# Performance work log

Hardware: AMD Instinct MI355X
Metric: run time of the kernel (lower is better)

## Reference

```python
import jax, jax.numpy as jnp
import numpy as np

B, H, S, D = 2, 16, 2048, 128

def setup_inputs() -> dict:
    key = jax.random.key(0)
    k1, k2, k3, k4 = jax.random.split(key, 4)
    queries = jax.random.normal(k1, (B, H, S, D), dtype=jnp.float32)
    keys = jax.random.normal(k2, (B, H, S, D), dtype=jnp.float32)
    values = jax.random.normal(k3, (B, H, S, D), dtype=jnp.float32)
    mask = jax.random.randint(k4, (B, 1, S, S), 0, 2).astype(jnp.int32)
    return {"queries": queries, "keys": keys, "values": values, "d_k": D, "mask": mask}

def reference(queries, keys, values, d_k, mask):
    # scores: [B, H, S, S]
    scale = 1.0 / jnp.sqrt(jnp.float32(d_k))
    scores = jnp.einsum('bhqd,bhkd->bhqk', queries, keys) * scale
    if mask is not None:
        scores = scores + (-1e9) * mask.astype(scores.dtype)
    weights = jax.nn.softmax(scores, axis=-1)
    out = jnp.einsum('bhqk,bhkd->bhqd', weights, values)
    return out
```

## Files before the change

kernel.cpp:

```cpp
#include <hip/hip_runtime.h>
#include <hip/hip_bf16.h>

#define BB 2
#define HH 16
#define SS 2048
#define DD 128
#define QBLK 128
#define KVBLK 64
#define NT (SS / KVBLK)
#define TILE_ELEMS (KVBLK * DD)

typedef __bf16 bf16x8 __attribute__((ext_vector_type(8)));
typedef __bf16 bf16x4 __attribute__((ext_vector_type(4)));
typedef float  f32x16 __attribute__((ext_vector_type(16)));

#define EXP2(x) __builtin_amdgcn_exp2f(x)
#define M2FIX 20.0f

__global__ __launch_bounds__(256)
void kimg_prep(const float* __restrict__ K, __bf16* __restrict__ Kd)
{
    #pragma unroll
    for (int i = 0; i < 4; ++i) {
        const int g   = blockIdx.x * 1024 + i * 256 + threadIdx.x;
        const int row = g >> 4;
        const int u   = (g & 15) ^ (row & 15);
        const float* src = K + (size_t)row * 128 + u * 8;
        float4 f0 = *(const float4*)src;
        float4 f1 = *(const float4*)(src + 4);
        bf16x8 h;
        h[0]=(__bf16)f0.x; h[1]=(__bf16)f0.y; h[2]=(__bf16)f0.z; h[3]=(__bf16)f0.w;
        h[4]=(__bf16)f1.x; h[5]=(__bf16)f1.y; h[6]=(__bf16)f1.z; h[7]=(__bf16)f1.w;
        *(bf16x8*)(Kd + (size_t)g * 8) = h;
    }
}

__global__ __launch_bounds__(256)
void vimg_prep(const float* __restrict__ V, __bf16* __restrict__ Vd)
{
    const int g    = blockIdx.x * 256 + threadIdx.x;
    const int tile = g >> 11;
    const int wu   = g & 2047;
    const int d    = wu >> 4;
    const int u    = wu & 15;
    const int s    = u ^ (d & 15);
    const int c    = s >> 2;
    const int hh   = (s >> 1) & 1;
    const int bb   = s & 1;
    const float* src = V + ((size_t)tile * 64 + c * 16 + 4 * hh + 8 * bb) * 128 + d;
    bf16x4 o;
    o[0] = (__bf16)src[0];
    o[1] = (__bf16)src[128];
    o[2] = (__bf16)src[256];
    o[3] = (__bf16)src[384];
    *(bf16x4*)(Vd + (size_t)g * 4) = o;
}

__global__ __launch_bounds__(256)
void mprep(const int* __restrict__ M, unsigned* __restrict__ mb)
{
    const int wid  = blockIdx.x * 4 + (threadIdx.x >> 6);
    const int lane = threadIdx.x & 63;
    const int kb   = wid & 31;
    const int q    = (wid >> 5) & 2047;
    const int b    = wid >> 16;
    const int mi   = M[((size_t)b * 2048 + q) * 2048 + kb * 64 + lane];
    const unsigned long long bal = __ballot(mi != 0);
    if (lane == 0) {
        uint2 st; st.x = (unsigned)bal; st.y = (unsigned)(bal >> 32);
        *(uint2*)&mb[((size_t)b * 2048 + q) * 64 + kb * 2] = st;
    }
}

__device__ __forceinline__ void load_lds16(const __bf16* g, __bf16* l) {
    __builtin_amdgcn_global_load_lds(
        (const __attribute__((address_space(1))) void*)g,
        (__attribute__((address_space(3))) void*)l, 16, 0, 0);
}

#define WAIT_VM(N)                                                             \
    do {                                                                       \
        asm volatile("s_waitcnt vmcnt(" #N ")" ::: "memory");                  \
        __builtin_amdgcn_sched_barrier(0);                                     \
    } while (0)

#define BAR() __builtin_amdgcn_s_barrier()

#define ISSUE_LDS(BUF)                                                         \
    do {                                                                       \
        _Pragma("unroll")                                                      \
        for (int i = 0; i < 4; ++i)                                            \
            load_lds16(kgp + i * 512, SMEM + (BUF) * 8192 + w * 2048 + i * 512); \
        _Pragma("unroll")                                                      \
        for (int i = 0; i < 4; ++i)                                            \
            load_lds16(vgp + i * 512, SMEM + 16384 + (BUF) * 8192 + w * 2048 + i * 512); \
        kgp += TILE_ELEMS;                                                     \
        vgp += TILE_ELEMS;                                                     \
    } while (0)

#define QK_TILE(BUF, S0, S1)                                                   \
    do {                                                                       \
        S0 = (f32x16)0.0f; S1 = (f32x16)0.0f;                                  \
        _Pragma("unroll")                                                      \
        for (int d0 = 0; d0 < 8; ++d0) {                                       \
            bf16x8 kf0 = *(const bf16x8*)(kp[d0] + (BUF) * 8192);              \
            bf16x8 kf1 = *(const bf16x8*)(kp[d0] + (BUF) * 8192 + 4096);       \
            S0 = __builtin_amdgcn_mfma_f32_32x32x16_bf16(kf0, qf[d0], S0, 0, 0, 0); \
            S1 = __builtin_amdgcn_mfma_f32_32x32x16_bf16(kf1, qf[d0], S1, 0, 0, 0); \
        }                                                                      \
    } while (0)

#define SM_TILE(S0, S1, MREG, PB)                                              \
    do {                                                                       \
        const unsigned w0 = (MREG).x >> sh4;                                   \
        const unsigned w1 = (MREG).y >> sh4;                                   \
        float rs = 0.0f;                                                       \
        _Pragma("unroll")                                                      \
        for (int c = 0; c < 4; ++c) {                                          \
            const unsigned wc = ((c & 2) ? w1 : w0) >> (16 * (c & 1));         \
            _Pragma("unroll")                                                  \
            for (int r = 0; r < 8; ++r) {                                      \
                float p = EXP2((((c & 2) ? S1 : S0)[(c & 1) * 8 + r]) - M2FIX);\
                p = (wc & (1u << ((r & 3) + 8 * (r >> 2)))) ? 0.0f : p;        \
                rs += p;                                                       \
                (PB)[c][r] = (__bf16)p;                                        \
            }                                                                  \
        }                                                                      \
        l_i += rs;                                                             \
    } while (0)

#define PV_TILE(BUF, PB)                                                       \
    do {                                                                       \
        _Pragma("unroll")                                                      \
        for (int c = 0; c < 4; ++c) {                                          \
            _Pragma("unroll")                                                  \
            for (int dd = 0; dd < 4; ++dd) {                                   \
                bf16x4 lo = *(const bf16x4*)(vp[c * 2]     + (BUF) * 8192 + dd * 2048); \
                bf16x4 hi = *(const bf16x4*)(vp[c * 2 + 1] + (BUF) * 8192 + dd * 2048); \
                bf16x8 va = __builtin_shufflevector(lo, hi, 0, 1, 2, 3, 4, 5, 6, 7); \
                o[dd] = __builtin_amdgcn_mfma_f32_32x32x16_bf16(va, (PB)[c], o[dd], 0, 0, 0); \
            }                                                                  \
        }                                                                      \
    } while (0)

#define BODY(BUFC, PB_USE, PB_FILL, MREG, DO_ISSUE)                            \
    do {                                                                       \
        WAIT_VM(0);                                                            \
        BAR();                                                                 \
        f32x16 s0, s1;                                                         \
        QK_TILE((BUFC) ^ 1, s0, s1);                                           \
        SM_TILE(s0, s1, MREG, PB_FILL);                                        \
        PV_TILE(BUFC, PB_USE);                                                 \
        BAR();                                                                 \
        if (DO_ISSUE) {                                                        \
            ISSUE_LDS(BUFC);                                                   \
            MREG = *(const uint2*)mp; mp += 2;                                 \
        }                                                                      \
    } while (0)

__global__ __launch_bounds__(256, 2)
void attn_fwd(const float* __restrict__ Q, const __bf16* __restrict__ Kimg,
              const __bf16* __restrict__ Vimg, const unsigned* __restrict__ MB,
              float* __restrict__ O)
{
    __shared__ __bf16 SMEM[4 * TILE_ELEMS];

    const int tid  = threadIdx.x;
    const int lane = tid & 63;
    const int ln31 = lane & 31;
    const int h    = lane >> 5;
    const int w    = tid >> 6;
    const int sh4  = 4 * h;

    const int bid = blockIdx.x;
    const int swz = (bid & 7) * 64 + (bid >> 3);
    const int qb  = swz & 15;
    const int bh  = swz >> 4;
    const int b   = bh >> 4;

    const float SC = 0.08838834764831845f * 1.4426950408889634f;

    const float* Qb = Q + (size_t)bh * SS * DD;
    float*       Ob = O + (size_t)bh * SS * DD;

    const int qrow = qb * QBLK + w * 32 + ln31;

    const __bf16*   kgp = Kimg + (size_t)bh * SS * DD + w * 2048 + lane * 8;
    const __bf16*   vgp = Vimg + (size_t)bh * SS * DD + w * 2048 + lane * 8;
    const unsigned* mp  = MB + ((size_t)b * 2048 + qrow) * 64;

    const int key = ln31 & 15;
    const __bf16* kp[8];
    #pragma unroll
    for (int j = 0; j < 8; ++j)
        kp[j] = SMEM + ln31 * 128 + (((j * 2 + h) ^ key) * 8);
    const __bf16* vp[8];
    #pragma unroll
    for (int u = 0; u < 8; ++u) {
        const int c = u >> 1, bb = u & 1;
        vp[u] = SMEM + 16384 + ln31 * 64 + (((c * 4 + 2 * h + bb) ^ key) * 4);
    }

    bf16x8 qf[8];
    {
        const float* qr = Qb + (size_t)qrow * DD + 8 * h;
        #pragma unroll
        for (int d0 = 0; d0 < 8; ++d0) {
            float4 f0 = *(const float4*)(qr + d0 * 16);
            float4 f1 = *(const float4*)(qr + d0 * 16 + 4);
            bf16x8 a;
            a[0]=(__bf16)(f0.x*SC); a[1]=(__bf16)(f0.y*SC);
            a[2]=(__bf16)(f0.z*SC); a[3]=(__bf16)(f0.w*SC);
            a[4]=(__bf16)(f1.x*SC); a[5]=(__bf16)(f1.y*SC);
            a[6]=(__bf16)(f1.z*SC); a[7]=(__bf16)(f1.w*SC);
            qf[d0] = a;
        }
    }
    __builtin_amdgcn_sched_barrier(0);

    f32x16 o[4];
    #pragma unroll
    for (int i = 0; i < 4; ++i) o[i] = (f32x16)0.0f;
    float l_i = 0.0f;

    bf16x8 pbE[4], pbO[4];
    uint2 mE, mO;

    ISSUE_LDS(0);
    uint2 mPro = *(const uint2*)mp; mp += 2;
    ISSUE_LDS(1);
    mE = *(const uint2*)mp; mp += 2;
    mO = *(const uint2*)mp; mp += 2;
    WAIT_VM(6);
    BAR();
    {
        f32x16 s0, s1;
        QK_TILE(0, s0, s1);
        SM_TILE(s0, s1, mPro, pbO);
    }

    #pragma unroll 1
    for (int t = 0; t < 30; t += 2) {
        BODY(0, pbO, pbE, mE, 1);
        BODY(1, pbE, pbO, mO, 1);
    }
    BODY(0, pbO, pbE, mE, 0);
    PV_TILE(1, pbE);

    l_i += __shfl_xor(l_i, 32);
    const float inv = (l_i > 0.0f) ? 1.0f / l_i : 0.0f;
    float* orow = Ob + (size_t)qrow * DD + 4 * h;
    #pragma unroll
    for (int dd = 0; dd < 4; ++dd) {
        #pragma unroll
        for (int rg = 0; rg < 4; ++rg) {
            float4 st;
            st.x = o[dd][rg*4+0] * inv; st.y = o[dd][rg*4+1] * inv;
            st.z = o[dd][rg*4+2] * inv; st.w = o[dd][rg*4+3] * inv;
            *(float4*)&orow[dd * 32 + rg * 8] = st;
        }
    }
}

extern "C" void kernel_launch(void* const* d_in, const int* in_sizes, int n_in,
                              void* d_out, int out_size, void* d_ws, size_t ws_size,
                              hipStream_t stream) {
    const float* Q = (const float*)d_in[0];
    const float* K = (const float*)d_in[1];
    const float* V = (const float*)d_in[2];
    const int*   M = (const int*)d_in[4];
    float*       O = (float*)d_out;

    const size_t NE = (size_t)BB * HH * SS * DD;
    __bf16*   Kimg = (__bf16*)d_ws;
    __bf16*   Vimg = Kimg + NE;
    unsigned* Mbit = (unsigned*)(Vimg + NE);

    kimg_prep<<<1024, 256, 0, stream>>>(K, Kimg);
    vimg_prep<<<8192, 256, 0, stream>>>(V, Vimg);
    mprep    <<<32768, 256, 0, stream>>>(M, Mbit);

    attn_fwd<<<BB * HH * (SS / QBLK), 256, 0, stream>>>(Q, Kimg, Vimg, Mbit, O);
}
```

Baseline: 130.2 us.

## Restructure attention loop into interleaved softmax-PV and QK phases with partial waits

Reorders the main loop so each step first does softmax fused with the P·V MFMAs for the previous tile, then computes QK scores for the next tile. Each chunk of P is fed into the PV MFMAs as soon as it is computed instead of being buffered for a whole tile. Full vmcnt(0) waits become partial waits, so LDS loads for later tiles can stay in flight. The goal is better overlap of exp/VALU work with MFMA and of global-to-LDS loads with compute, and fewer live P registers. The risk is that wrong vmcnt counts could race with the async LDS loads.

Result: no change. 129.6 us (-0.5%).

```diff
diff --git a/kernel.cpp b/kernel.cpp
--- a/kernel.cpp
+++ b/kernel.cpp
@@ -98,19 +98,7 @@
         vgp += TILE_ELEMS;                                                     \
     } while (0)
 
-#define QK_TILE(BUF, S0, S1)                                                   \
-    do {                                                                       \
-        S0 = (f32x16)0.0f; S1 = (f32x16)0.0f;                                  \
-        _Pragma("unroll")                                                      \
-        for (int d0 = 0; d0 < 8; ++d0) {                                       \
-            bf16x8 kf0 = *(const bf16x8*)(kp[d0] + (BUF) * 8192);              \
-            bf16x8 kf1 = *(const bf16x8*)(kp[d0] + (BUF) * 8192 + 4096);       \
-            S0 = __builtin_amdgcn_mfma_f32_32x32x16_bf16(kf0, qf[d0], S0, 0, 0, 0); \
-            S1 = __builtin_amdgcn_mfma_f32_32x32x16_bf16(kf1, qf[d0], S1, 0, 0, 0); \
-        }                                                                      \
-    } while (0)
-
-#define SM_TILE(S0, S1, MREG, PB)                                              \
+#define SMPV(PBUF, MREG)                                                       \
     do {                                                                       \
         const unsigned w0 = (MREG).x >> sh4;                                   \
         const unsigned w1 = (MREG).y >> sh4;                                   \
@@ -118,42 +106,47 @@
         _Pragma("unroll")                                                      \
         for (int c = 0; c < 4; ++c) {                                          \
             const unsigned wc = ((c & 2) ? w1 : w0) >> (16 * (c & 1));         \
+            bf16x8 pb;                                                         \
             _Pragma("unroll")                                                  \
             for (int r = 0; r < 8; ++r) {                                      \
-                float p = EXP2((((c & 2) ? S1 : S0)[(c & 1) * 8 + r]) - M2FIX);\
+                float p = EXP2((((c & 2) ? sQ1 : sQ0)[(c & 1) * 8 + r]) - M2FIX);\
                 p = (wc & (1u << ((r & 3) + 8 * (r >> 2)))) ? 0.0f : p;        \
                 rs += p;                                                       \
-                (PB)[c][r] = (__bf16)p;                                        \
+                pb[r] = (__bf16)p;                                             \
+            }                                                                  \
+            _Pragma("unroll")                                                  \
+            for (int dd = 0; dd < 4; ++dd) {                                   \
+                bf16x4 lo = *(const bf16x4*)(vp[c * 2]     + (PBUF) * 8192 + dd * 2048); \
+                bf16x4 hi = *(const bf16x4*)(vp[c * 2 + 1] + (PBUF) * 8192 + dd * 2048); \
+                bf16x8 va = __builtin_shufflevector(lo, hi, 0, 1, 2, 3, 4, 5, 6, 7); \
+                o[dd] = __builtin_amdgcn_mfma_f32_32x32x16_bf16(va, pb, o[dd], 0, 0, 0); \
             }                                                                  \
         }                                                                      \
         l_i += rs;                                                             \
     } while (0)
 
-#define PV_TILE(BUF, PB)                                                       \
-    do {                                                                       \
-        _Pragma("unroll")                                                      \
-        for (int c = 0; c < 4; ++c) {                                          \
-            _Pragma("unroll")                                                  \
-            for (int dd = 0; dd < 4; ++dd) {                                   \
-                bf16x4 lo = *(const bf16x4*)(vp[c * 2]     + (BUF) * 8192 + dd * 2048); \
-                bf16x4 hi = *(const bf16x4*)(vp[c * 2 + 1] + (BUF) * 8192 + dd * 2048); \
-                bf16x8 va = __builtin_shufflevector(lo, hi, 0, 1, 2, 3, 4, 5, 6, 7); \
-                o[dd] = __builtin_amdgcn_mfma_f32_32x32x16_bf16(va, (PB)[c], o[dd], 0, 0, 0); \
-            }                                                                  \
+#define QK_PH(KBUF)                                                            \
+    do {                                                                       \
+        sQ0 = (f32x16)0.0f; sQ1 = (f32x16)0.0f;                                \
+        _Pragma("unroll")                                                      \
+        for (int d0 = 0; d0 < 8; ++d0) {                                       \
+            bf16x8 kf0 = *(const bf16x8*)(kp[d0] + (KBUF) * 8192);             \
+            bf16x8 kf1 = *(const bf16x8*)(kp[d0] + (KBUF) * 8192 + 4096);      \
+            sQ0 = __builtin_amdgcn_mfma_f32_32x32x16_bf16(kf0, qf[d0], sQ0, 0, 0, 0); \
+            sQ1 = __builtin_amdgcn_mfma_f32_32x32x16_bf16(kf1, qf[d0], sQ1, 0, 0, 0); \
         }                                                                      \
     } while (0)
 
-#define BODY(BUFC, PB_USE, PB_FILL, MREG, DO_ISSUE)                            \
-    do {                                                                       \
-        WAIT_VM(0);                                                            \
+#define BODY(P, MREG, DO_ISSUE)                                                \
+    do {                                                                       \
+        WAIT_VM(9);                                                            \
         BAR();                                                                 \
-        f32x16 s0, s1;                                                         \
-        QK_TILE((BUFC) ^ 1, s0, s1);                                           \
-        SM_TILE(s0, s1, MREG, PB_FILL);                                        \
-        PV_TILE(BUFC, PB_USE);                                                 \
+        SMPV((P) ^ 1, MREG);                                                   \
+        WAIT_VM(5);                                                            \
         BAR();                                                                 \
+        QK_PH(P);                                                              \
         if (DO_ISSUE) {                                                        \
-            ISSUE_LDS(BUFC);                                                   \
+            ISSUE_LDS((P) ^ 1);                                                \
             MREG = *(const uint2*)mp; mp += 2;                                 \
         }                                                                      \
     } while (0)
@@ -223,29 +216,24 @@
     for (int i = 0; i < 4; ++i) o[i] = (f32x16)0.0f;
     float l_i = 0.0f;
 
-    bf16x8 pbE[4], pbO[4];
-    uint2 mE, mO;
-
-    ISSUE_LDS(0);
-    uint2 mPro = *(const uint2*)mp; mp += 2;
-    ISSUE_LDS(1);
-    mE = *(const uint2*)mp; mp += 2;
-    mO = *(const uint2*)mp; mp += 2;
-    WAIT_VM(6);
+    f32x16 sQ0, sQ1;
+    uint2 mA, mB2;
+
+    ISSUE_LDS(0); mA  = *(const uint2*)mp; mp += 2;
+    ISSUE_LDS(1); mB2 = *(const uint2*)mp; mp += 2;
+    WAIT_VM(9);
     BAR();
-    {
-        f32x16 s0, s1;
-        QK_TILE(0, s0, s1);
-        SM_TILE(s0, s1, mPro, pbO);
-    }
+    QK_PH(0);
 
     #pragma unroll 1
-    for (int t = 0; t < 30; t += 2) {
-        BODY(0, pbO, pbE, mE, 1);
-        BODY(1, pbE, pbO, mO, 1);
-    }
-    BODY(0, pbO, pbE, mE, 0);
-    PV_TILE(1, pbE);
+    for (int i = 0; i < 15; ++i) {
+        BODY(1, mA, 1);
+        BODY(0, mB2, 1);
+    }
+    BODY(1, mA, 0);
+    WAIT_VM(0);
+    BAR();
+    SMPV(1, mB2);
 
     l_i += __shfl_xor(l_i, 32);
     const float inv = (l_i > 0.0f) ? 1.0f / l_i : 0.0f;
```
